# Kernel optimization log

Hardware: AMD Instinct MI355X
Metric: run time of the kernel (lower is better)

Reference implementation:

```python
import jax, jax.numpy as jnp
import numpy as np

B, S, D, H = 4, 2048, 1024, 16
HD = D // H


def setup_inputs() -> dict:
    key = jax.random.key(0)
    ks = jax.random.split(key, 12)
    inp = {
        'query': jax.random.normal(ks[0], (B, S, D), jnp.float32),
        'key': jax.random.normal(ks[1], (B, S, D), jnp.float32),
        'value': jax.random.normal(ks[2], (B, S, D), jnp.float32),
        'mask': jnp.ones((B, 1, 1, S), jnp.bool_),
        # nn.Linear weights are [out, in]; y = x @ W.T + b
        'Wq': jax.random.normal(ks[3], (D, D), jnp.float32) * 0.02,
        'bq': jnp.zeros((D,), jnp.float32),
        'Wk': jax.random.normal(ks[4], (D, D), jnp.float32) * 0.02,
        'bk': jnp.zeros((D,), jnp.float32),
        'Wv': jax.random.normal(ks[5], (D, D), jnp.float32) * 0.02,
        'bv': jnp.zeros((D,), jnp.float32),
        'Wo': jax.random.normal(ks[6], (D, D), jnp.float32) * 0.02,
        'bo': jnp.zeros((D,), jnp.float32),
    }
    return inp


def reference(query, key, value, mask, Wq, bq, Wk, bk, Wv, bv, Wo, bo):
    scale = 1.0 / np.sqrt(HD).astype(np.float32)

    def proj(x, W, b):
        # [B,S,D] -> [B,H,S,HD]
        y = x @ W.T + b
        return y.reshape(B, S, H, HD).transpose(0, 2, 1, 3)

    q = proj(query, Wq, bq)
    k = proj(key, Wk, bk)
    v = proj(value, Wv, bv)
    # scores: [B,H,S,S]
    scores = jnp.einsum('bhqd,bhkd->bhqk', q, k) * scale
    scores = jnp.where(mask, scores, -jnp.inf)
    attn = jax.nn.softmax(scores, axis=-1)  # dropout p=0 in eval
    ctx = jnp.einsum('bhqk,bhkd->bhqd', attn, v)  # [B,H,S,HD]
    ctx = ctx.transpose(0, 2, 1, 3).reshape(B, S, D)
    return ctx @ Wo.T + bo
```

## Files before the change

### kernel.cpp

```cpp
#include <hip/hip_runtime.h>
#include <hip/hip_bf16.h>

#define LOG2E 1.4426950408889634f

typedef __attribute__((ext_vector_type(8))) short short8;
typedef __attribute__((ext_vector_type(4))) short short4v;
typedef __attribute__((ext_vector_type(4))) float f32x4;

__device__ __forceinline__ short f2bf(float f) {
    __hip_bfloat16 h = __float2bfloat16(f);
    short s;
    __builtin_memcpy(&s, &h, 2);
    return s;
}

__device__ __forceinline__ void gl_lds16(const void* g, void* l) {
    __builtin_amdgcn_global_load_lds(
        (const __attribute__((address_space(1))) unsigned int*)g,
        (__attribute__((address_space(3))) unsigned int*)l,
        16, 0, 0);
}

__global__ __launch_bounds__(256) void cvt3(
    const float* __restrict__ a, const float* __restrict__ b,
    const float* __restrict__ c, short* __restrict__ oa,
    short* __restrict__ ob, short* __restrict__ oc, int n8)
{
    int i = blockIdx.x * 256 + threadIdx.x;
    if (i >= n8) return;
    const float* in = blockIdx.y == 0 ? a : (blockIdx.y == 1 ? b : c);
    short* out = blockIdx.y == 0 ? oa : (blockIdx.y == 1 ? ob : oc);
    float4 v0 = ((const float4*)in)[2 * i];
    float4 v1 = ((const float4*)in)[2 * i + 1];
    short8 s = { f2bf(v0.x), f2bf(v0.y), f2bf(v0.z), f2bf(v0.w),
                 f2bf(v1.x), f2bf(v1.y), f2bf(v1.z), f2bf(v1.w) };
    *(short8*)(out + 8 * (size_t)i) = s;
}

__global__ __launch_bounds__(256) void cvt4(
    const float* __restrict__ a, const float* __restrict__ b,
    const float* __restrict__ c, const float* __restrict__ d,
    short* __restrict__ oa, short* __restrict__ ob,
    short* __restrict__ oc, short* __restrict__ od, int n8)
{
    int i = blockIdx.x * 256 + threadIdx.x;
    if (i >= n8) return;
    const float* in = blockIdx.y == 0 ? a : (blockIdx.y == 1 ? b :
                      (blockIdx.y == 2 ? c : d));
    short* out = blockIdx.y == 0 ? oa : (blockIdx.y == 1 ? ob :
                 (blockIdx.y == 2 ? oc : od));
    float4 v0 = ((const float4*)in)[2 * i];
    float4 v1 = ((const float4*)in)[2 * i + 1];
    short8 s = { f2bf(v0.x), f2bf(v0.y), f2bf(v0.z), f2bf(v0.w),
                 f2bf(v1.x), f2bf(v1.y), f2bf(v1.z), f2bf(v1.w) };
    *(short8*)(out + 8 * (size_t)i) = s;
}

template<bool OUT_BF16>
__global__ __launch_bounds__(256) void gemm_bt_bf16(
    const short* __restrict__ A, const short* __restrict__ W,
    const float* __restrict__ bias, void* __restrict__ Cptr,
    int M, int N, int K)
{
    __shared__ short As[128 * 64];
    __shared__ short Bs[128 * 64];
    const int tid = threadIdx.x;
    const int wave = tid >> 6, lane = tid & 63;
    const int quad = lane >> 4, l16 = lane & 15;
    const int wm = (wave >> 1) * 64, wn = (wave & 1) * 64;
    const int bm0 = blockIdx.y * 128, bn0 = blockIdx.x * 128;
    const int rowA = lane >> 3, chunk = (lane & 7) * 8;

    const short* Ab = A + (size_t)bm0 * K;
    const short* Wb = W + (size_t)bn0 * K;

    f32x4 acc[4][4] = {};

    for (int kt = 0; kt < K; kt += 64) {
        #pragma unroll
        for (int i = 0; i < 4; ++i) {
            int r0 = wave * 32 + i * 8;
            gl_lds16(Ab + (size_t)(r0 + rowA) * K + kt + chunk, As + r0 * 64);
            gl_lds16(Wb + (size_t)(r0 + rowA) * K + kt + chunk, Bs + r0 * 64);
        }
        __syncthreads();

        #pragma unroll
        for (int h = 0; h < 2; ++h) {
            short8 af[4], bf[4];
            #pragma unroll
            for (int mi = 0; mi < 4; ++mi)
                af[mi] = *(const short8*)(As + (wm + mi * 16 + l16) * 64 + h * 32 + quad * 8);
            #pragma unroll
            for (int ni = 0; ni < 4; ++ni)
                bf[ni] = *(const short8*)(Bs + (wn + ni * 16 + l16) * 64 + h * 32 + quad * 8);
            #pragma unroll
            for (int mi = 0; mi < 4; ++mi)
                #pragma unroll
                for (int ni = 0; ni < 4; ++ni)
                    acc[mi][ni] = __builtin_amdgcn_mfma_f32_16x16x32_bf16(
                        af[mi], bf[ni], acc[mi][ni], 0, 0, 0);
        }
        __syncthreads();
    }

    #pragma unroll
    for (int ni = 0; ni < 4; ++ni) {
        int n = bn0 + wn + ni * 16 + l16;
        float bb = bias[n];
        #pragma unroll
        for (int mi = 0; mi < 4; ++mi)
            #pragma unroll
            for (int r = 0; r < 4; ++r) {
                int m = bm0 + wm + mi * 16 + quad * 4 + r;
                float v = acc[mi][ni][r] + bb;
                if constexpr (OUT_BF16)
                    ((short*)Cptr)[(size_t)m * N + n] = f2bf(v);
                else
                    ((float*)Cptr)[(size_t)m * N + n] = v;
            }
    }
}

__global__ __launch_bounds__(256) void transpose_v(
    const short* __restrict__ Vb, short* __restrict__ VT)
{
    const int S = 2048, D = 1024;
    __shared__ short T[64 * 64];
    const int tid = threadIdx.x;
    const int s0 = blockIdx.x * 64;
    const int h  = blockIdx.y;
    const int b  = blockIdx.z;

    #pragma unroll
    for (int it = 0; it < 2; ++it) {
        int c = tid + it * 256;
        int s = c >> 3, cd = c & 7;
        short8 v = *(const short8*)(Vb + ((size_t)(b * S + s0 + s)) * D + h * 64 + cd * 8);
        int chunk = cd ^ ((s >> 3) & 7);
        *(short8*)(T + s * 64 + chunk * 8) = v;
    }
    __syncthreads();
    #pragma unroll
    for (int it = 0; it < 2; ++it) {
        int c = tid + it * 256;
        int d = c >> 3, so = (c & 7) * 8;
        short8 v;
        #pragma unroll
        for (int i = 0; i < 8; ++i) {
            int s = so + i;
            int chunk = (d >> 3) ^ ((s >> 3) & 7);
            v[i] = T[s * 64 + chunk * 8 + (d & 7)];
        }
        *(short8*)(VT + ((size_t)((b * 16 + h) * 64 + d)) * S + s0 + so) = v;
    }
}

__global__ __launch_bounds__(256) void flash_attn(
    const short* __restrict__ Q, const short* __restrict__ Kb,
    const short* __restrict__ VT, const int* __restrict__ mask,
    short* __restrict__ Ctx)
{
    const int S = 2048, D = 1024;
    __shared__ short Ks[64 * 64];
    __shared__ short Vs[64 * 64];
    __shared__ short Ps[4][32 * 72];

    const int tid = threadIdx.x;
    const int wave = tid >> 6, lane = tid & 63;
    const int quad = lane >> 4, l16 = lane & 15;
    const int q0 = blockIdx.x * 128 + wave * 32;
    const int head = blockIdx.y, b = blockIdx.z;
    const size_t qbase  = ((size_t)(b * S)) * D + head * 64;
    const size_t vtbase = ((size_t)((b * 16 + head) * 64)) * S;
    const int rowA = lane >> 3, chunk = (lane & 7) * 8;

    short8 qf[2][2];
    #pragma unroll
    for (int qi = 0; qi < 2; ++qi)
        #pragma unroll
        for (int h = 0; h < 2; ++h)
            qf[qi][h] = *(const short8*)(Q + qbase + (size_t)(q0 + qi * 16 + l16) * D + h * 32 + quad * 8);

    f32x4 o[2][4] = {};
    float ls[2][4] = {};

    const int* mrow = mask + (size_t)b * S;
    short* Pw = Ps[wave];

    for (int kt = 0; kt < S; kt += 64) {
        __syncthreads();
        {
            int r0 = wave * 16;
            gl_lds16(Kb + qbase + (size_t)(kt + r0 + rowA) * D + chunk, Ks + r0 * 64);
            gl_lds16(Kb + qbase + (size_t)(kt + r0 + 8 + rowA) * D + chunk, Ks + (r0 + 8) * 64);
            gl_lds16(VT + vtbase + (size_t)(r0 + rowA) * S + kt + chunk, Vs + r0 * 64);
            gl_lds16(VT + vtbase + (size_t)(r0 + 8 + rowA) * S + kt + chunk, Vs + (r0 + 8) * 64);
        }
        __syncthreads();

        float p[2][4][4];
        #pragma unroll
        for (int t = 0; t < 4; ++t) {
            short8 kf0 = *(const short8*)(Ks + (t * 16 + l16) * 64 + quad * 8);
            short8 kf1 = *(const short8*)(Ks + (t * 16 + l16) * 64 + 32 + quad * 8);
            bool okt = mrow[kt + t * 16 + l16] != 0;
            #pragma unroll
            for (int qi = 0; qi < 2; ++qi) {
                f32x4 a = {};
                a = __builtin_amdgcn_mfma_f32_16x16x32_bf16(qf[qi][0], kf0, a, 0, 0, 0);
                a = __builtin_amdgcn_mfma_f32_16x16x32_bf16(qf[qi][1], kf1, a, 0, 0, 0);
                #pragma unroll
                for (int r = 0; r < 4; ++r) {
                    float sc = okt ? a[r] * 0.125f : -1e30f;
                    float pv = __builtin_amdgcn_exp2f(sc * LOG2E);
                    p[qi][t][r] = pv;
                    ls[qi][r] += pv;
                }
            }
        }

        #pragma unroll
        for (int qi = 0; qi < 2; ++qi)
            #pragma unroll
            for (int t = 0; t < 4; ++t)
                #pragma unroll
                for (int r = 0; r < 4; ++r)
                    Pw[(qi * 16 + quad * 4 + r) * 72 + t * 16 + l16] = f2bf(p[qi][t][r]);

        #pragma unroll
        for (int h = 0; h < 2; ++h) {
            short8 pa0 = *(const short8*)(Pw + l16 * 72 + h * 32 + quad * 8);
            short8 pa1 = *(const short8*)(Pw + (16 + l16) * 72 + h * 32 + quad * 8);
            #pragma unroll
            for (int nt = 0; nt < 4; ++nt) {
                short8 bv = *(const short8*)(Vs + (nt * 16 + l16) * 64 + h * 32 + quad * 8);
                o[0][nt] = __builtin_amdgcn_mfma_f32_16x16x32_bf16(pa0, bv, o[0][nt], 0, 0, 0);
                o[1][nt] = __builtin_amdgcn_mfma_f32_16x16x32_bf16(pa1, bv, o[1][nt], 0, 0, 0);
            }
        }
    }

    #pragma unroll
    for (int qi = 0; qi < 2; ++qi)
        #pragma unroll
        for (int r = 0; r < 4; ++r) {
            float v = ls[qi][r];
            #pragma unroll
            for (int off = 1; off < 16; off <<= 1)
                v += __shfl_xor(v, off, 64);
            ls[qi][r] = 1.0f / v;
        }

    #pragma unroll
    for (int qi = 0; qi < 2; ++qi)
        #pragma unroll
        for (int nt = 0; nt < 4; ++nt)
            #pragma unroll
            for (int r = 0; r < 4; ++r) {
                float v = o[qi][nt][r] * ls[qi][r];
                Ctx[qbase + (size_t)(q0 + qi * 16 + quad * 4 + r) * D + nt * 16 + l16] = f2bf(v);
            }
}

extern "C" void kernel_launch(void* const* d_in, const int* in_sizes, int n_in,
                              void* d_out, int out_size, void* d_ws, size_t ws_size,
                              hipStream_t stream) {
    const int B = 4, S = 2048, D = 1024, H = 16;
    const int M = B * S;
    const size_t MD = (size_t)M * D;

    const float* q_in = (const float*)d_in[0];
    const float* k_in = (const float*)d_in[1];
    const float* v_in = (const float*)d_in[2];
    const int* mask = (const int*)d_in[3];
    const float* Wq = (const float*)d_in[4];
    const float* bq = (const float*)d_in[5];
    const float* Wk = (const float*)d_in[6];
    const float* bk = (const float*)d_in[7];
    const float* Wv = (const float*)d_in[8];
    const float* bv = (const float*)d_in[9];
    const float* Wo = (const float*)d_in[10];
    const float* bo = (const float*)d_in[11];

    short* S1 = (short*)d_ws;
    short* S2 = S1 + MD;
    short* S3 = S2 + MD;
    short* S4 = S3 + MD;
    short* wqb = S4 + MD;
    short* wkb = wqb + (size_t)D * D;
    short* wvb = wkb + (size_t)D * D;
    short* wob = wvb + (size_t)D * D;

    short *qbf = S1, *kbf = S2, *vbf = S3;
    short *Qb = S4, *Kb = S1, *Vb = S2, *VT = S3, *Ctx = S2;

    dim3 blk(256);
    int n8_in = (int)(MD / 8);
    int n8_w  = D * D / 8;
    cvt3<<<dim3((n8_in + 255) / 256, 3), blk, 0, stream>>>(
        q_in, k_in, v_in, qbf, kbf, vbf, n8_in);
    cvt4<<<dim3((n8_w + 255) / 256, 4), blk, 0, stream>>>(
        Wq, Wk, Wv, Wo, wqb, wkb, wvb, wob, n8_w);

    dim3 g1(D / 128, M / 128);
    gemm_bt_bf16<true><<<g1, blk, 0, stream>>>(qbf, wqb, bq, Qb, M, D, D);
    gemm_bt_bf16<true><<<g1, blk, 0, stream>>>(kbf, wkb, bk, Kb, M, D, D);
    gemm_bt_bf16<true><<<g1, blk, 0, stream>>>(vbf, wvb, bv, Vb, M, D, D);

    transpose_v<<<dim3(S / 64, H, B), blk, 0, stream>>>(Vb, VT);

    dim3 g2(S / 128, H, B);
    flash_attn<<<g2, blk, 0, stream>>>(Qb, Kb, VT, mask, Ctx);

    gemm_bt_bf16<false><<<g1, blk, 0, stream>>>(Ctx, wob, bo, (float*)d_out, M, D, D);
}
```

Before: 446.8 us.

## Swizzle LDS tiles, batch QKV projections into one launch, fuse score scaling

```diff
diff --git a/kernel.cpp b/kernel.cpp
--- a/kernel.cpp
+++ b/kernel.cpp
@@ -2,9 +2,9 @@
 #include <hip/hip_bf16.h>
 
 #define LOG2E 1.4426950408889634f
+#define SCLOG (0.125f * 1.4426950408889634f)
 
 typedef __attribute__((ext_vector_type(8))) short short8;
-typedef __attribute__((ext_vector_type(4))) short short4v;
 typedef __attribute__((ext_vector_type(4))) float f32x4;
 
 __device__ __forceinline__ short f2bf(float f) {
@@ -56,11 +56,16 @@
     *(short8*)(out + 8 * (size_t)i) = s;
 }
 
-template<bool OUT_BF16>
+template<int NZ, bool OUT_BF16>
 __global__ __launch_bounds__(256) void gemm_bt_bf16(
-    const short* __restrict__ A, const short* __restrict__ W,
-    const float* __restrict__ bias, void* __restrict__ Cptr,
-    int M, int N, int K)
+    const short* __restrict__ A0, const short* __restrict__ A1,
+    const short* __restrict__ A2,
+    const short* __restrict__ W0, const short* __restrict__ W1,
+    const short* __restrict__ W2,
+    const float* __restrict__ b0, const float* __restrict__ b1,
+    const float* __restrict__ b2,
+    short* __restrict__ C0, short* __restrict__ C1, short* __restrict__ C2,
+    void* __restrict__ Cf, int M, int N, int K)
 {
     __shared__ short As[128 * 64];
     __shared__ short Bs[128 * 64];
@@ -69,7 +74,19 @@
     const int quad = lane >> 4, l16 = lane & 15;
     const int wm = (wave >> 1) * 64, wn = (wave & 1) * 64;
     const int bm0 = blockIdx.y * 128, bn0 = blockIdx.x * 128;
-    const int rowA = lane >> 3, chunk = (lane & 7) * 8;
+    const int rowA = lane >> 3;
+    const int chunkS = (((lane & 7) ^ rowA) * 8);
+    const int rsw = (l16 & 7);
+
+    const short* A; const short* W; const float* bias; short* Cb;
+    if constexpr (NZ == 3) {
+        A    = blockIdx.z == 0 ? A0 : (blockIdx.z == 1 ? A1 : A2);
+        W    = blockIdx.z == 0 ? W0 : (blockIdx.z == 1 ? W1 : W2);
+        bias = blockIdx.z == 0 ? b0 : (blockIdx.z == 1 ? b1 : b2);
+        Cb   = blockIdx.z == 0 ? C0 : (blockIdx.z == 1 ? C1 : C2);
+    } else {
+        A = A0; W = W0; bias = b0; Cb = C0;
+    }
 
     const short* Ab = A + (size_t)bm0 * K;
     const short* Wb = W + (size_t)bn0 * K;
@@ -80,20 +97,21 @@
         #pragma unroll
         for (int i = 0; i < 4; ++i) {
             int r0 = wave * 32 + i * 8;
-            gl_lds16(Ab + (size_t)(r0 + rowA) * K + kt + chunk, As + r0 * 64);
-            gl_lds16(Wb + (size_t)(r0 + rowA) * K + kt + chunk, Bs + r0 * 64);
+            gl_lds16(Ab + (size_t)(r0 + rowA) * K + kt + chunkS, As + r0 * 64);
+            gl_lds16(Wb + (size_t)(r0 + rowA) * K + kt + chunkS, Bs + r0 * 64);
         }
         __syncthreads();
 
         #pragma unroll
         for (int h = 0; h < 2; ++h) {
+            const int slot = ((h * 4 + quad) ^ rsw) * 8;
             short8 af[4], bf[4];
             #pragma unroll
             for (int mi = 0; mi < 4; ++mi)
-                af[mi] = *(const short8*)(As + (wm + mi * 16 + l16) * 64 + h * 32 + quad * 8);
+                af[mi] = *(const short8*)(As + (wm + mi * 16 + l16) * 64 + slot);
             #pragma unroll
             for (int ni = 0; ni < 4; ++ni)
-                bf[ni] = *(const short8*)(Bs + (wn + ni * 16 + l16) * 64 + h * 32 + quad * 8);
+                bf[ni] = *(const short8*)(Bs + (wn + ni * 16 + l16) * 64 + slot);
             #pragma unroll
             for (int mi = 0; mi < 4; ++mi)
                 #pragma unroll
@@ -115,9 +133,9 @@
                 int m = bm0 + wm + mi * 16 + quad * 4 + r;
                 float v = acc[mi][ni][r] + bb;
                 if constexpr (OUT_BF16)
-                    ((short*)Cptr)[(size_t)m * N + n] = f2bf(v);
+                    Cb[(size_t)m * N + n] = f2bf(v);
                 else
-                    ((float*)Cptr)[(size_t)m * N + n] = v;
+                    ((float*)Cf)[(size_t)m * N + n] = v;
             }
     }
 }
@@ -173,7 +191,9 @@
     const int head = blockIdx.y, b = blockIdx.z;
     const size_t qbase  = ((size_t)(b * S)) * D + head * 64;
     const size_t vtbase = ((size_t)((b * 16 + head) * 64)) * S;
-    const int rowA = lane >> 3, chunk = (lane & 7) * 8;
+    const int rowA = lane >> 3;
+    const int chunkS = (((lane & 7) ^ rowA) * 8);
+    const int rsw = (l16 & 7);
 
     short8 qf[2][2];
     #pragma unroll
@@ -187,24 +207,26 @@
 
     const int* mrow = mask + (size_t)b * S;
     short* Pw = Ps[wave];
+    const int slot0 = (quad ^ rsw) * 8;
+    const int slot1 = ((4 + quad) ^ rsw) * 8;
 
     for (int kt = 0; kt < S; kt += 64) {
         __syncthreads();
         {
             int r0 = wave * 16;
-            gl_lds16(Kb + qbase + (size_t)(kt + r0 + rowA) * D + chunk, Ks + r0 * 64);
-            gl_lds16(Kb + qbase + (size_t)(kt + r0 + 8 + rowA) * D + chunk, Ks + (r0 + 8) * 64);
-            gl_lds16(VT + vtbase + (size_t)(r0 + rowA) * S + kt + chunk, Vs + r0 * 64);
-            gl_lds16(VT + vtbase + (size_t)(r0 + 8 + rowA) * S + kt + chunk, Vs + (r0 + 8) * 64);
+            gl_lds16(Kb + qbase + (size_t)(kt + r0 + rowA) * D + chunkS, Ks + r0 * 64);
+            gl_lds16(Kb + qbase + (size_t)(kt + r0 + 8 + rowA) * D + chunkS, Ks + (r0 + 8) * 64);
+            gl_lds16(VT + vtbase + (size_t)(r0 + rowA) * S + kt + chunkS, Vs + r0 * 64);
+            gl_lds16(VT + vtbase + (size_t)(r0 + 8 + rowA) * S + kt + chunkS, Vs + (r0 + 8) * 64);
         }
         __syncthreads();
 
         float p[2][4][4];
         #pragma unroll
         for (int t = 0; t < 4; ++t) {
-            short8 kf0 = *(const short8*)(Ks + (t * 16 + l16) * 64 + quad * 8);
-            short8 kf1 = *(const short8*)(Ks + (t * 16 + l16) * 64 + 32 + quad * 8);
-            bool okt = mrow[kt + t * 16 + l16] != 0;
+            short8 kf0 = *(const short8*)(Ks + (t * 16 + l16) * 64 + slot0);
+            short8 kf1 = *(const short8*)(Ks + (t * 16 + l16) * 64 + slot1);
+            float mb = mrow[kt + t * 16 + l16] != 0 ? 0.f : -1e30f;
             #pragma unroll
             for (int qi = 0; qi < 2; ++qi) {
                 f32x4 a = {};
@@ -212,8 +234,7 @@
                 a = __builtin_amdgcn_mfma_f32_16x16x32_bf16(qf[qi][1], kf1, a, 0, 0, 0);
                 #pragma unroll
                 for (int r = 0; r < 4; ++r) {
-                    float sc = okt ? a[r] * 0.125f : -1e30f;
-                    float pv = __builtin_amdgcn_exp2f(sc * LOG2E);
+                    float pv = __builtin_amdgcn_exp2f(__builtin_fmaf(a[r], SCLOG, mb));
                     p[qi][t][r] = pv;
                     ls[qi][r] += pv;
                 }
@@ -230,11 +251,12 @@
 
         #pragma unroll
         for (int h = 0; h < 2; ++h) {
+            const int vslot = ((h * 4 + quad) ^ rsw) * 8;
             short8 pa0 = *(const short8*)(Pw + l16 * 72 + h * 32 + quad * 8);
             short8 pa1 = *(const short8*)(Pw + (16 + l16) * 72 + h * 32 + quad * 8);
             #pragma unroll
             for (int nt = 0; nt < 4; ++nt) {
-                short8 bv = *(const short8*)(Vs + (nt * 16 + l16) * 64 + h * 32 + quad * 8);
+                short8 bv = *(const short8*)(Vs + (nt * 16 + l16) * 64 + vslot);
                 o[0][nt] = __builtin_amdgcn_mfma_f32_16x16x32_bf16(pa0, bv, o[0][nt], 0, 0, 0);
                 o[1][nt] = __builtin_amdgcn_mfma_f32_16x16x32_bf16(pa1, bv, o[1][nt], 0, 0, 0);
             }
@@ -303,15 +325,22 @@
     cvt4<<<dim3((n8_w + 255) / 256, 4), blk, 0, stream>>>(
         Wq, Wk, Wv, Wo, wqb, wkb, wvb, wob, n8_w);
 
-    dim3 g1(D / 128, M / 128);
-    gemm_bt_bf16<true><<<g1, blk, 0, stream>>>(qbf, wqb, bq, Qb, M, D, D);
-    gemm_bt_bf16<true><<<g1, blk, 0, stream>>>(kbf, wkb, bk, Kb, M, D, D);
-    gemm_bt_bf16<true><<<g1, blk, 0, stream>>>(vbf, wvb, bv, Vb, M, D, D);
-
-    transpose_v<<<dim3(S / 64, H, B), blk, 0, stream>>>(Vb, VT);
+    short* S5 = wob + (size_t)D * D;
+    short* S6 = S5 + MD;
+    short* Kb2 = S5;
+    short* Vb2 = S6;
+    dim3 g1(D / 128, M / 128, 3);
+    gemm_bt_bf16<3, true><<<g1, blk, 0, stream>>>(
+        qbf, kbf, vbf, wqb, wkb, wvb, bq, bk, bv,
+        Qb, Kb2, Vb2, nullptr, M, D, D);
+
+    transpose_v<<<dim3(S / 64, H, B), blk, 0, stream>>>(Vb2, VT);
 
     dim3 g2(S / 128, H, B);
-    flash_attn<<<g2, blk, 0, stream>>>(Qb, Kb, VT, mask, Ctx);
-
-    gemm_bt_bf16<false><<<g1, blk, 0, stream>>>(Ctx, wob, bo, (float*)d_out, M, D, D);
-}
+    flash_attn<<<g2, blk, 0, stream>>>(Qb, Kb2, VT, mask, Ctx);
+
+    dim3 g3(D / 128, M / 128, 1);
+    gemm_bt_bf16<1, false><<<g3, blk, 0, stream>>>(
+        Ctx, nullptr, nullptr, wob, nullptr, nullptr, bo, nullptr, nullptr,
+        nullptr, nullptr, nullptr, (float*)d_out, M, D, D);
+}
```

Measured after the change: 382.2 us. 1.17x faster.
